# Performance work log

Hardware: AMD Instinct MI355X
Metric: run time of the kernel (lower is better)

Reference implementation:

```python
import jax, jax.numpy as jnp
import numpy as np

B = 16384
N_NARR = 128
N_SUB = 1024
K = N_SUB // N_NARR  # narrative i -> subnarratives [i*K, (i+1)*K)
GAMMA = 2.0
NW, SW, HW = 1.0, 1.0, 0.5  # narrative/subnarrative/hierarchy weights


def setup_inputs() -> dict:
    key = jax.random.key(0)
    k1, k2, k3, k4 = jax.random.split(key, 4)
    return {
        "narrative_logits": jax.random.normal(k1, (B, N_NARR), jnp.float32),
        "subnarrative_logits": jax.random.normal(k2, (B, N_SUB), jnp.float32),
        "narrative_labels": jax.random.randint(k3, (B, N_NARR), 0, 2, jnp.int32),
        "subnarrative_labels": jax.random.randint(k4, (B, N_SUB), 0, 2, jnp.int32),
    }


def _weighted_bce(logits, labels, pos_weight):
    # BCEWithLogits with pos_weight: pw*y*softplus(-x) + (1-y)*softplus(x)
    return pos_weight * labels * jax.nn.softplus(-logits) + (1.0 - labels) * jax.nn.softplus(logits)


def reference(narrative_logits, subnarrative_logits, narrative_labels, subnarrative_labels):
    nl = narrative_labels.astype(jnp.float32)
    sl = subnarrative_labels.astype(jnp.float32)
    b = narrative_logits.shape[0]

    # class-balanced pos_weights, clamped to [1, 50]
    npw = jnp.clip((1.0 - nl).sum(0) / (nl.sum(0) + 1e-6), 1.0, 50.0)
    spw = jnp.clip((1.0 - sl).sum(0) / (sl.sum(0) + 1e-6), 1.0, 50.0)

    narrative_loss = _weighted_bce(narrative_logits, nl, npw).mean()

    # ragged subnarrative loss, vectorized: groups of K subnarrs per narrative.
    # per-(sample, positive-narrative) mean BCE over the group, averaged over
    # the number of valid (sample, narrative) pairs -- same math as the loop.
    sub_bce = _weighted_bce(subnarrative_logits, sl, spw).reshape(b, N_NARR, K)
    per_group = sub_bce.mean(-1)              # [B, N_NARR]
    pos = nl                                   # positive-narrative mask [B, N_NARR]
    valid_count = pos.sum()
    subnarrative_loss = jnp.where(
        valid_count > 0, (per_group * pos).sum() / jnp.maximum(valid_count, 1.0), 0.0)

    # hierarchy consistency: relu(max subnarr prob - narr prob) over positives
    nprob = jax.nn.sigmoid(narrative_logits)
    sprob = jax.nn.sigmoid(subnarrative_logits)
    grp_max = sprob.reshape(b, N_NARR, K).max(-1)  # [B, N_NARR]
    hierarchy_loss = (jax.nn.relu(grp_max - nprob) * pos).sum() / b

    # focal terms (mean over all elements)
    nf = ((1.0 - nprob) ** GAMMA * nl * jax.nn.log_sigmoid(narrative_logits)).mean()
    sf = ((1.0 - sprob) ** GAMMA * sl * jax.nn.log_sigmoid(subnarrative_logits)).mean()

    total = (NW * (narrative_loss - 0.1 * nf)
             + SW * (subnarrative_loss - 0.1 * sf)
             + HW * hierarchy_loss)
    return total
```

## Files before the change

kernel.cpp:

```cpp
#include <hip/hip_runtime.h>


#define BDIM 256
#define NROWS 16384
#define NNARR 128
#define NSUB 1024
#define RPB 8
#define NBLOCKS (NROWS / RPB)

#define WS_AN    0
#define WS_CN    128
#define WS_NSUM  256
#define WS_AS    384
#define WS_CS    1408
#define WS_SSUM  2432
#define WS_FN    3456
#define WS_FS    3457
#define WS_HIER  3458
#define WS_FLOATS 3459
#define CSTRIDE  3472
#define CHUNK    64
#define NTMP     32

__device__ __forceinline__ void bce_pieces(float x, float& sp_p, float& sp_m, float& sig) {
    float a = fabsf(x);
    float e = __expf(-a);
    float l = __logf(1.0f + e);
    sp_p = fmaxf(x, 0.0f) + l;
    sp_m = sp_p - x;
    float inv = __builtin_amdgcn_rcpf(1.0f + e);
    sig = (x >= 0.0f) ? inv : e * inv;
}

__device__ __forceinline__ void emit4(float* dst, float a, float b, float c, float d, int excl) {
    if (excl) {
        *(float4*)dst = make_float4(a, b, c, d);
    } else {
        atomicAdd(dst + 0, a); atomicAdd(dst + 1, b);
        atomicAdd(dst + 2, c); atomicAdd(dst + 3, d);
    }
}

__global__ __launch_bounds__(BDIM, 8) void ncl_main(
    const float* __restrict__ nlog, const float* __restrict__ slog,
    const int*   __restrict__ nlab, const int*   __restrict__ slab,
    float* __restrict__ ws, int ncopies, int excl)
{
    __shared__ float sred[BDIM][13];
    __shared__ float pss_s[RPB * NNARR];
    __shared__ float ssc[4][3];

    const int t  = threadIdx.x;
    const int r0 = blockIdx.x * RPB;
    float* const cw = ws + (size_t)(blockIdx.x % ncopies) * CSTRIDE;

    float fn = 0.f, fs = 0.f, hier = 0.f;

    {
        const int base = r0 * NNARR + 4 * t;
        const float4 xs = *(const float4*)(nlog + base);
        const int4   ys = *(const int4*)  (nlab + base);
        const float xv[4] = {xs.x, xs.y, xs.z, xs.w};
        const float yv[4] = {(float)ys.x, (float)ys.y, (float)ys.z, (float)ys.w};
        float An[4], Cn[4], ns[4], ps[4];
        #pragma unroll
        for (int j = 0; j < 4; ++j) {
            float sp_p, sp_m, sig;
            bce_pieces(xv[j], sp_p, sp_m, sig);
            float y = yv[j];
            An[j] = y * sp_m;
            Cn[j] = (1.0f - y) * sp_p;
            ns[j] = y;
            float om = 1.0f - sig;
            fn += om * om * y * (-sp_m);
            ps[j] = (y != 0.0f) ? sig : -sig;
        }
        *(float4*)&pss_s[(t >> 5) * NNARR + 4 * (t & 31)] =
            make_float4(ps[0], ps[1], ps[2], ps[3]);
        #pragma unroll
        for (int j = 0; j < 4; ++j) {
            sred[t][j] = An[j]; sred[t][4 + j] = Cn[j]; sred[t][8 + j] = ns[j];
        }
    }
    __syncthreads();
    if (t < 32) {
        float a[12];
        #pragma unroll
        for (int j = 0; j < 12; ++j) a[j] = sred[t][j];
        #pragma unroll
        for (int s = 1; s < 8; ++s)
            #pragma unroll
            for (int j = 0; j < 12; ++j) a[j] += sred[t + 32 * s][j];
        emit4(cw + WS_AN   + 4 * t, a[0], a[1], a[2],  a[3],  excl);
        emit4(cw + WS_CN   + 4 * t, a[4], a[5], a[6],  a[7],  excl);
        emit4(cw + WS_NSUM + 4 * t, a[8], a[9], a[10], a[11], excl);
    }

    const int g = t >> 1;
    float As[4] = {0,0,0,0}, Cs[4] = {0,0,0,0}, ss[4] = {0,0,0,0};
    #pragma unroll 4
    for (int i = 0; i < RPB; ++i) {
        const int r = r0 + i;
        const float  pv   = pss_s[i * NNARR + g];
        const float  posv = (__float_as_uint(pv) >> 31) ? 0.0f : 1.0f;
        const float4 xs = *(const float4*)(slog + r * NSUB + 4 * t);
        const int4   ys = *(const int4*)  (slab + r * NSUB + 4 * t);

        const float xv[4] = {xs.x, xs.y, xs.z, xs.w};
        const float yv[4] = {(float)ys.x, (float)ys.y, (float)ys.z, (float)ys.w};
        float mymax = 0.0f;
        #pragma unroll
        for (int j = 0; j < 4; ++j) {
            float sp_p, sp_m, sig;
            bce_pieces(xv[j], sp_p, sp_m, sig);
            float y = yv[j];
            As[j] += posv * y * sp_m;
            Cs[j] += posv * (1.0f - y) * sp_p;
            ss[j] += y;
            float om = 1.0f - sig;
            fs += om * om * y * (-sp_m);
            mymax = fmaxf(mymax, sig);
        }
        float gmax = fmaxf(mymax, __shfl_xor(mymax, 1, 64));
        if ((t & 1) == 0)
            hier += fmaxf(gmax - fabsf(pv), 0.0f) * posv;
    }

    emit4(cw + WS_AS   + 4 * t, As[0], As[1], As[2], As[3], excl);
    emit4(cw + WS_CS   + 4 * t, Cs[0], Cs[1], Cs[2], Cs[3], excl);
    emit4(cw + WS_SSUM + 4 * t, ss[0], ss[1], ss[2], ss[3], excl);

    #pragma unroll
    for (int off = 32; off; off >>= 1) {
        fn   += __shfl_down(fn,   off, 64);
        fs   += __shfl_down(fs,   off, 64);
        hier += __shfl_down(hier, off, 64);
    }
    if ((t & 63) == 0) {
        int w = t >> 6;
        ssc[w][0] = fn; ssc[w][1] = fs; ssc[w][2] = hier;
    }
    __syncthreads();
    if (t == 0) {
        float a = 0.f, b = 0.f, c = 0.f;
        #pragma unroll
        for (int w = 0; w < 4; ++w) { a += ssc[w][0]; b += ssc[w][1]; c += ssc[w][2]; }
        if (excl) {
            cw[WS_FN] = a; cw[WS_FS] = b; cw[WS_HIER] = c;
        } else {
            atomicAdd(cw + WS_FN, a); atomicAdd(cw + WS_FS, b); atomicAdd(cw + WS_HIER, c);
        }
    }
}

__global__ __launch_bounds__(256) void ncl_reduce1(const float* __restrict__ ws,
                                                   float* __restrict__ tmp,
                                                   int ncopies)
{
    const int e4 = blockIdx.x * 256 + threadIdx.x;
    if (e4 >= CSTRIDE / 4) return;
    const int c0 = blockIdx.y * CHUNK;
    const int c1 = min(c0 + CHUNK, ncopies);
    float4 s = make_float4(0.f, 0.f, 0.f, 0.f);
    for (int c = c0; c < c1; ++c) {
        float4 v = *(const float4*)(ws + (size_t)c * CSTRIDE + 4 * e4);
        s.x += v.x; s.y += v.y; s.z += v.z; s.w += v.w;
    }
    *(float4*)(tmp + (size_t)blockIdx.y * CSTRIDE + 4 * e4) = s;
}

__global__ __launch_bounds__(1024) void ncl_final(const float* __restrict__ tmp,
                                                  float* __restrict__ out, int nchunks)
{
    __shared__ float sr[3][16];
    __shared__ float sc3[3];
    const int t = threadIdx.x;
    const float Bf = (float)NROWS;

    float s_as = 0.f, s_cs = 0.f, s_ss = 0.f;
    for (int c = 0; c < nchunks; ++c) {
        const float* b = tmp + (size_t)c * CSTRIDE;
        s_as += b[WS_AS + t]; s_cs += b[WS_CS + t]; s_ss += b[WS_SSUM + t];
    }
    float s_an = 0.f, s_cn = 0.f, s_ns = 0.f;
    if (t < NNARR) {
        for (int c = 0; c < nchunks; ++c) {
            const float* b = tmp + (size_t)c * CSTRIDE;
            s_an += b[WS_AN + t]; s_cn += b[WS_CN + t]; s_ns += b[WS_NSUM + t];
        }
    }
    if (t < 3) {
        float s = 0.f;
        for (int c = 0; c < nchunks; ++c) s += tmp[(size_t)c * CSTRIDE + WS_FN + t];
        sc3[t] = s;
    }

    float spw = fminf(fmaxf((Bf - s_ss) / (s_ss + 1e-6f), 1.0f), 50.0f);
    float sub_part = spw * s_as + s_cs;
    float narr_part = 0.f, valid_part = 0.f;
    if (t < NNARR) {
        float npw = fminf(fmaxf((Bf - s_ns) / (s_ns + 1e-6f), 1.0f), 50.0f);
        narr_part  = npw * s_an + s_cn;
        valid_part = s_ns;
    }

    #pragma unroll
    for (int off = 32; off; off >>= 1) {
        sub_part   += __shfl_down(sub_part,   off, 64);
        narr_part  += __shfl_down(narr_part,  off, 64);
        valid_part += __shfl_down(valid_part, off, 64);
    }
    if ((t & 63) == 0) {
        int w = t >> 6;
        sr[0][w] = sub_part; sr[1][w] = narr_part; sr[2][w] = valid_part;
    }
    __syncthreads();
    if (t == 0) {
        float sub_tot = 0.f, narr_tot = 0.f, valid = 0.f;
        #pragma unroll
        for (int i = 0; i < 16; ++i) { sub_tot += sr[0][i]; narr_tot += sr[1][i]; valid += sr[2][i]; }

        float narrative_loss = narr_tot / (Bf * (float)NNARR);
        float sub_loss = (valid > 0.0f) ? (sub_tot * (1.0f / 8.0f)) / fmaxf(valid, 1.0f) : 0.0f;
        float nf = sc3[0] / (Bf * (float)NNARR);
        float sf = sc3[1] / (Bf * (float)NSUB);
        float hier_loss = sc3[2] / Bf;

        out[0] = (narrative_loss - 0.1f * nf)
               + (sub_loss       - 0.1f * sf)
               + 0.5f * hier_loss;
    }
}

extern "C" void kernel_launch(void* const* d_in, const int* in_sizes, int n_in,
                              void* d_out, int out_size, void* d_ws, size_t ws_size,
                              hipStream_t stream) {
    const float* nlog = (const float*)d_in[0];
    const float* slog = (const float*)d_in[1];
    const int*   nlab = (const int*)d_in[2];
    const int*   slab = (const int*)d_in[3];
    float* ws  = (float*)d_ws;
    float* out = (float*)d_out;

    long avail = (long)(ws_size / 4);
    long nc = avail / CSTRIDE - NTMP;
    int ncopies = (int)(nc < 1 ? 1 : (nc > NBLOCKS ? NBLOCKS : nc));
    int excl = (ncopies == NBLOCKS) ? 1 : 0;
    float* tmp = (nc < 1) ? ws : ws + (size_t)ncopies * CSTRIDE;
    int nchunks = (ncopies + CHUNK - 1) / CHUNK;

    if (!excl)
        hipMemsetAsync(ws, 0, (size_t)ncopies * CSTRIDE * sizeof(float), stream);

    ncl_main<<<NBLOCKS, BDIM, 0, stream>>>(nlog, slog, nlab, slab, ws, ncopies, excl);

    dim3 g1((CSTRIDE / 4 + 255) / 256, nchunks);
    ncl_reduce1<<<g1, 256, 0, stream>>>(ws, tmp, ncopies);
    ncl_final<<<1, 1024, 0, stream>>>(tmp, out, nchunks);
}
```

Measured before the change: 217.3 us.

## Double rows per block and software-pipeline subnarrative loads in chunks of four

```diff
diff --git a/kernel.cpp b/kernel.cpp
--- a/kernel.cpp
+++ b/kernel.cpp
@@ -5,7 +5,7 @@
 #define NROWS 16384
 #define NNARR 128
 #define NSUB 1024
-#define RPB 8
+#define RPB 16
 #define NBLOCKS (NROWS / RPB)
 
 #define WS_AN    0
@@ -20,7 +20,7 @@
 #define WS_FLOATS 3459
 #define CSTRIDE  3472
 #define CHUNK    64
-#define NTMP     32
+#define NTMP     16
 
 __device__ __forceinline__ void bce_pieces(float x, float& sp_p, float& sp_m, float& sig) {
     float a = fabsf(x);
@@ -41,7 +41,7 @@
     }
 }
 
-__global__ __launch_bounds__(BDIM, 8) void ncl_main(
+__global__ __launch_bounds__(BDIM, 4) void ncl_main(
     const float* __restrict__ nlog, const float* __restrict__ slog,
     const int*   __restrict__ nlab, const int*   __restrict__ slab,
     float* __restrict__ ws, int ncopies, int excl)
@@ -57,26 +57,31 @@
     float fn = 0.f, fs = 0.f, hier = 0.f;
 
     {
-        const int base = r0 * NNARR + 4 * t;
-        const float4 xs = *(const float4*)(nlog + base);
-        const int4   ys = *(const int4*)  (nlab + base);
-        const float xv[4] = {xs.x, xs.y, xs.z, xs.w};
-        const float yv[4] = {(float)ys.x, (float)ys.y, (float)ys.z, (float)ys.w};
-        float An[4], Cn[4], ns[4], ps[4];
-        #pragma unroll
-        for (int j = 0; j < 4; ++j) {
-            float sp_p, sp_m, sig;
-            bce_pieces(xv[j], sp_p, sp_m, sig);
-            float y = yv[j];
-            An[j] = y * sp_m;
-            Cn[j] = (1.0f - y) * sp_p;
-            ns[j] = y;
-            float om = 1.0f - sig;
-            fn += om * om * y * (-sp_m);
-            ps[j] = (y != 0.0f) ? sig : -sig;
-        }
-        *(float4*)&pss_s[(t >> 5) * NNARR + 4 * (t & 31)] =
-            make_float4(ps[0], ps[1], ps[2], ps[3]);
+        float An[4] = {0,0,0,0}, Cn[4] = {0,0,0,0}, ns[4] = {0,0,0,0};
+        #pragma unroll
+        for (int i = 0; i < 2; ++i) {
+            const int base = r0 * NNARR + 4 * (i * BDIM + t);
+            const float4 xs = *(const float4*)(nlog + base);
+            const int4   ys = *(const int4*)  (nlab + base);
+            const float xv[4] = {xs.x, xs.y, xs.z, xs.w};
+            const float yv[4] = {(float)ys.x, (float)ys.y, (float)ys.z, (float)ys.w};
+            float ps[4];
+            #pragma unroll
+            for (int j = 0; j < 4; ++j) {
+                float sp_p, sp_m, sig;
+                bce_pieces(xv[j], sp_p, sp_m, sig);
+                float y = yv[j];
+                An[j] += y * sp_m;
+                Cn[j] += (1.0f - y) * sp_p;
+                ns[j] += y;
+                float om = 1.0f - sig;
+                fn += om * om * y * (-sp_m);
+                ps[j] = (y != 0.0f) ? sig : -sig;
+            }
+            const int row = i * 8 + (t >> 5);
+            *(float4*)&pss_s[row * NNARR + 4 * (t & 31)] =
+                make_float4(ps[0], ps[1], ps[2], ps[3]);
+        }
         #pragma unroll
         for (int j = 0; j < 4; ++j) {
             sred[t][j] = An[j]; sred[t][4 + j] = Cn[j]; sred[t][8 + j] = ns[j];
@@ -97,33 +102,56 @@
     }
 
     const int g = t >> 1;
+    const float* sx = slog + (size_t)r0 * NSUB + 4 * t;
+    const int*   sy = slab + (size_t)r0 * NSUB + 4 * t;
     float As[4] = {0,0,0,0}, Cs[4] = {0,0,0,0}, ss[4] = {0,0,0,0};
-    #pragma unroll 4
-    for (int i = 0; i < RPB; ++i) {
-        const int r = r0 + i;
-        const float  pv   = pss_s[i * NNARR + g];
-        const float  posv = (__float_as_uint(pv) >> 31) ? 0.0f : 1.0f;
-        const float4 xs = *(const float4*)(slog + r * NSUB + 4 * t);
-        const int4   ys = *(const int4*)  (slab + r * NSUB + 4 * t);
-
-        const float xv[4] = {xs.x, xs.y, xs.z, xs.w};
-        const float yv[4] = {(float)ys.x, (float)ys.y, (float)ys.z, (float)ys.w};
-        float mymax = 0.0f;
-        #pragma unroll
-        for (int j = 0; j < 4; ++j) {
-            float sp_p, sp_m, sig;
-            bce_pieces(xv[j], sp_p, sp_m, sig);
-            float y = yv[j];
-            As[j] += posv * y * sp_m;
-            Cs[j] += posv * (1.0f - y) * sp_p;
-            ss[j] += y;
-            float om = 1.0f - sig;
-            fs += om * om * y * (-sp_m);
-            mymax = fmaxf(mymax, sig);
-        }
-        float gmax = fmaxf(mymax, __shfl_xor(mymax, 1, 64));
-        if ((t & 1) == 0)
-            hier += fmaxf(gmax - fabsf(pv), 0.0f) * posv;
+
+    float4 xb[4]; int4 yb[4];
+    #pragma unroll
+    for (int i = 0; i < 4; ++i) {
+        xb[i] = *(const float4*)(sx + (size_t)i * NSUB);
+        yb[i] = *(const int4*)  (sy + (size_t)i * NSUB);
+    }
+
+    #pragma unroll
+    for (int c = 0; c < 4; ++c) {
+        float4 xn[4]; int4 yn[4];
+        if (c < 3) {
+            #pragma unroll
+            for (int i = 0; i < 4; ++i) {
+                xn[i] = *(const float4*)(sx + (size_t)((c + 1) * 4 + i) * NSUB);
+                yn[i] = *(const int4*)  (sy + (size_t)((c + 1) * 4 + i) * NSUB);
+            }
+        }
+        #pragma unroll
+        for (int i = 0; i < 4; ++i) {
+            const int row = c * 4 + i;
+            const float pv   = pss_s[row * NNARR + g];
+            const float posv = (__float_as_uint(pv) >> 31) ? 0.0f : 1.0f;
+            const float xv[4] = {xb[i].x, xb[i].y, xb[i].z, xb[i].w};
+            const float yv[4] = {(float)yb[i].x, (float)yb[i].y,
+                                 (float)yb[i].z, (float)yb[i].w};
+            float mymax = 0.0f;
+            #pragma unroll
+            for (int j = 0; j < 4; ++j) {
+                float sp_p, sp_m, sig;
+                bce_pieces(xv[j], sp_p, sp_m, sig);
+                float y = yv[j];
+                As[j] += posv * y * sp_m;
+                Cs[j] += posv * (1.0f - y) * sp_p;
+                ss[j] += y;
+                float om = 1.0f - sig;
+                fs += om * om * y * (-sp_m);
+                mymax = fmaxf(mymax, sig);
+            }
+            float gmax = fmaxf(mymax, __shfl_xor(mymax, 1, 64));
+            if ((t & 1) == 0)
+                hier += fmaxf(gmax - fabsf(pv), 0.0f) * posv;
+        }
+        if (c < 3) {
+            #pragma unroll
+            for (int i = 0; i < 4; ++i) { xb[i] = xn[i]; yb[i] = yn[i]; }
+        }
     }
 
     emit4(cw + WS_AS   + 4 * t, As[0], As[1], As[2], As[3], excl);
```

After: 346.5 us. 1.59x slower.
